# Kernel optimization log

Hardware: AMD Instinct MI355X
Metric: run time of the kernel (lower is better)

Reference implementation:

```python
import jax, jax.numpy as jnp
import numpy as np

U = 100000   # num_users
I = 100000   # num_items
D = 64       # latent_dim_rec
L = 3        # lightGCN_n_layers
E = 6400000  # number of nonzeros in the sparse adjacency
B = 16384    # batch of (user, item) pairs
N = U + I


def setup_inputs() -> dict:
    key = jax.random.key(0)
    ks = jax.random.split(key, 11)
    return {
        "user_emb": 0.1 * jax.random.normal(ks[0], (U, D), dtype=jnp.float32),
        "item_emb": 0.1 * jax.random.normal(ks[1], (I, D), dtype=jnp.float32),
        "symptom_emb": 0.1 * jax.random.normal(ks[2], (U, D), dtype=jnp.float32),
        "herb_emb": 0.1 * jax.random.normal(ks[3], (I, D), dtype=jnp.float32),
        "user_lw": jax.random.uniform(ks[4], (L + 1,), dtype=jnp.float32),
        "item_lw": jax.random.uniform(ks[5], (L + 1,), dtype=jnp.float32),
        # symmetric-normalized adjacency values are small positive numbers
        "edge_val": jax.random.uniform(ks[6], (E,), dtype=jnp.float32) / 32.0,
        "edge_row": jax.random.randint(ks[7], (E,), 0, N, dtype=jnp.int32),
        "edge_col": jax.random.randint(ks[8], (E,), 0, N, dtype=jnp.int32),
        "users": jax.random.randint(ks[9], (B,), 0, U, dtype=jnp.int32),
        "items": jax.random.randint(ks[10], (B,), 0, I, dtype=jnp.int32),
    }


def _computer(user_emb, item_emb, symptom_emb, herb_emb, user_lw, item_lw,
              edge_val, edge_row, edge_col):
    # layer-0 semantic fusion
    a0 = jax.nn.sigmoid(user_lw[0])
    b0 = jax.nn.sigmoid(item_lw[0])
    u = a0 * user_emb + (1.0 - a0) * symptom_emb
    it = b0 * item_emb + (1.0 - b0) * herb_emb
    all_emb = jnp.concatenate([u, it], axis=0)  # [N, D]
    acc = all_emb  # running sum over layers (mean taken at the end)
    for layer in range(1, L + 1):
        # SpMM: A @ all_emb via gather + segment_sum over edge list
        msg = edge_val[:, None] * all_emb[edge_col]          # [E, D]
        all_emb = jax.ops.segment_sum(msg, edge_row, num_segments=N)
        a = jax.nn.sigmoid(user_lw[layer])
        b = jax.nn.sigmoid(item_lw[layer])
        cu = a * all_emb[:U] + (1.0 - a) * symptom_emb
        ci = b * all_emb[U:] + (1.0 - b) * herb_emb
        all_emb = jnp.concatenate([cu, ci], axis=0)
        acc = acc + all_emb
    light_out = acc / (L + 1)   # mean over stacked layer outputs
    return light_out[:U], light_out[U:]


def reference(user_emb, item_emb, symptom_emb, herb_emb, user_lw, item_lw,
              edge_val, edge_row, edge_col, users, items):
    all_users, all_items = _computer(user_emb, item_emb, symptom_emb, herb_emb,
                                     user_lw, item_lw, edge_val, edge_row, edge_col)
    users_emb = all_users[users]   # [B, D]
    items_emb = all_items[items]   # [B, D]
    gamma = jnp.sum(users_emb * items_emb, axis=1)  # [B]
    return gamma
```

## Files before the change

### kernel.cpp

```cpp
#include <hip/hip_runtime.h>

constexpr int U_N = 100000;
constexpr int I_N = 100000;
constexpr int D   = 64;
constexpr int NL  = 3;
constexpr int NN  = U_N + I_N;
constexpr long long NDLL = (long long)NN * D;
constexpr long long ND4  = NDLL / 4;
constexpr long long UD4  = (long long)U_N * D / 4;

constexpr int BKT_SHIFT = 10;
constexpr int BKT_W     = 1024;
constexpr int NBKT      = (NN + BKT_W - 1) / BKT_W;
constexpr int ABLK      = 1024;

typedef float f32x2 __attribute__((ext_vector_type(2)));

__device__ __forceinline__ float sigmoidf_(float x) {
    return 1.0f / (1.0f + expf(-x));
}

__device__ __forceinline__ float bf2f(unsigned short b) {
    return __uint_as_float((unsigned int)b << 16);
}
__device__ __forceinline__ float bf_lo(unsigned int u) {
    return __uint_as_float(u << 16);
}
__device__ __forceinline__ float bf_hi(unsigned int u) {
    return __uint_as_float(u & 0xFFFF0000u);
}
__device__ __forceinline__ f32x2 bfpair(unsigned int u) {
    f32x2 r;
    r.x = __uint_as_float(u << 16);
    r.y = __uint_as_float(u & 0xFFFF0000u);
    return r;
}
__device__ __forceinline__ unsigned short f2bf(float f) {
    unsigned int u = __float_as_uint(f);
    u += 0x7FFFu + ((u >> 16) & 1u);
    return (unsigned short)(u >> 16);
}
__device__ __forceinline__ unsigned int pack2bf(float lo, float hi) {
    return (unsigned int)f2bf(lo) | ((unsigned int)f2bf(hi) << 16);
}

__global__ void fuse0_bf16_kernel(const float* __restrict__ user_emb,
                                  const float* __restrict__ item_emb,
                                  const float* __restrict__ symptom_emb,
                                  const float* __restrict__ herb_emb,
                                  const float* __restrict__ user_lw,
                                  const float* __restrict__ item_lw,
                                  unsigned short* __restrict__ e0b) {
    long long idx = (long long)blockIdx.x * blockDim.x + threadIdx.x;
    if (idx >= ND4) return;
    float a0 = sigmoidf_(user_lw[0]);
    float b0 = sigmoidf_(item_lw[0]);
    float4 e, s;
    float w;
    if (idx < UD4) {
        e = ((const float4*)user_emb)[idx];
        s = ((const float4*)symptom_emb)[idx];
        w = a0;
    } else {
        long long j = idx - UD4;
        e = ((const float4*)item_emb)[j];
        s = ((const float4*)herb_emb)[j];
        w = b0;
    }
    ushort4 rb;
    rb.x = f2bf(w * e.x + (1.0f - w) * s.x);
    rb.y = f2bf(w * e.y + (1.0f - w) * s.y);
    rb.z = f2bf(w * e.z + (1.0f - w) * s.z);
    rb.w = f2bf(w * e.w + (1.0f - w) * s.w);
    ((ushort4*)e0b)[idx] = rb;
}

__global__ void zero_bcnt_kernel(int* __restrict__ bucket_cnt) {
    int i = blockIdx.x * blockDim.x + threadIdx.x;
    if (i < NBKT) bucket_cnt[i] = 0;
}

__global__ void bucket_hist_kernel(const int* __restrict__ edge_row,
                                   int* __restrict__ bucket_cnt,
                                   int E, int chunk) {
    __shared__ int h[NBKT];
    int tid = threadIdx.x;
    for (int i = tid; i < NBKT; i += blockDim.x) h[i] = 0;
    __syncthreads();
    int s = blockIdx.x * chunk;
    int eend = min(E, s + chunk);
    for (int e = s + tid; e < eend; e += blockDim.x)
        atomicAdd(&h[edge_row[e] >> BKT_SHIFT], 1);
    __syncthreads();
    for (int i = tid; i < NBKT; i += blockDim.x) {
        int c = h[i];
        if (c) atomicAdd(&bucket_cnt[i], c);
    }
}

__global__ void scan_bkt_kernel(const int* __restrict__ bucket_cnt,
                                int* __restrict__ boff,
                                int* __restrict__ cursorA, int E) {
    __shared__ int sm[256];
    int tid = threadIdx.x;
    int x = (tid < NBKT) ? bucket_cnt[tid] : 0;
    sm[tid] = x;
    __syncthreads();
    for (int off = 1; off < 256; off <<= 1) {
        int t = (tid >= off) ? sm[tid - off] : 0;
        __syncthreads();
        sm[tid] += t;
        __syncthreads();
    }
    if (tid < NBKT) {
        int excl = sm[tid] - x;
        boff[tid] = excl;
        cursorA[tid] = excl;
    }
    if (tid == 0) boff[NBKT] = E;
}

__global__ void bin_scatter_kernel(const float* __restrict__ edge_val,
                                   const int*   __restrict__ edge_row,
                                   const int*   __restrict__ edge_col,
                                   int* __restrict__ cursorA,
                                   int2* __restrict__ binned,
                                   int E, int chunk) {
    __shared__ int h[NBKT];
    int tid = threadIdx.x;
    for (int i = tid; i < NBKT; i += blockDim.x) h[i] = 0;
    __syncthreads();
    int s = blockIdx.x * chunk;
    int eend = min(E, s + chunk);
    for (int e = s + tid; e < eend; e += blockDim.x)
        atomicAdd(&h[edge_row[e] >> BKT_SHIFT], 1);
    __syncthreads();
    for (int i = tid; i < NBKT; i += blockDim.x) {
        int c = h[i];
        if (c) h[i] = atomicAdd(&cursorA[i], c);
    }
    __syncthreads();
    for (int e = s + tid; e < eend; e += blockDim.x) {
        int r = edge_row[e];
        int b = r >> BKT_SHIFT;
        int pos = atomicAdd(&h[b], 1);
        binned[pos] = make_int2(__float_as_int(edge_val[e]),
                                edge_col[e] | ((r & (BKT_W - 1)) << 18));
    }
}

__global__ void bucket_to_csr_kernel(const int2* __restrict__ binned,
                                     const int*  __restrict__ boff,
                                     int*  __restrict__ row_ptr,
                                     int2* __restrict__ sorted, int E) {
    int b = blockIdx.x;
    int start = boff[b];
    int end   = boff[b + 1];
    __shared__ int rc[BKT_W];
    __shared__ int sm[BKT_W];
    int tid = threadIdx.x;
    rc[tid] = 0;
    __syncthreads();
    for (int e = start + tid; e < end; e += blockDim.x)
        atomicAdd(&rc[(unsigned)binned[e].y >> 18], 1);
    __syncthreads();
    int x = rc[tid];
    sm[tid] = x;
    __syncthreads();
    for (int off = 1; off < BKT_W; off <<= 1) {
        int t = (tid >= off) ? sm[tid - off] : 0;
        __syncthreads();
        sm[tid] += t;
        __syncthreads();
    }
    int excl = sm[tid] - x;
    int gidx = (b << BKT_SHIFT) + tid;
    if (gidx <= NN) row_ptr[gidx] = start + excl;
    __syncthreads();
    rc[tid] = excl;
    __syncthreads();
    for (int e = start + tid; e < end; e += blockDim.x) {
        int2 a = binned[e];
        int rl = (unsigned)a.y >> 18;
        int pos = start + atomicAdd(&rc[rl], 1);
        sorted[pos] = make_int2(a.x, a.y & 0x3FFFF);
    }
}

__device__ __forceinline__ void csr_row_sum(const int2* __restrict__ sorted,
                                            const uint4* __restrict__ src16,
                                            int start, int end,
                                            int g, int p, f32x2 s[4]) {
    f32x2 s0[4], s1[4];
    #pragma unroll
    for (int j = 0; j < 4; ++j) {
        s0[j] = (f32x2){0.f, 0.f};
        s1[j] = (f32x2){0.f, 0.f};
    }
    int e = start;
    for (; e + 16 <= end; e += 16) {
        int2 a0 = sorted[e + g];
        int2 a1 = sorted[e + 8 + g];
        uint4 q0 = src16[((size_t)(unsigned)a0.y << 3) + p];
        uint4 q1 = src16[((size_t)(unsigned)a1.y << 3) + p];
        f32x2 v0; v0.x = __int_as_float(a0.x); v0.y = v0.x;
        f32x2 v1; v1.x = __int_as_float(a1.x); v1.y = v1.x;
        s0[0] += v0 * bfpair(q0.x);
        s0[1] += v0 * bfpair(q0.y);
        s0[2] += v0 * bfpair(q0.z);
        s0[3] += v0 * bfpair(q0.w);
        s1[0] += v1 * bfpair(q1.x);
        s1[1] += v1 * bfpair(q1.y);
        s1[2] += v1 * bfpair(q1.z);
        s1[3] += v1 * bfpair(q1.w);
    }
    for (; e < end; e += 8) {
        int idx = e + g;
        int2 a = (idx < end) ? sorted[idx] : make_int2(0, 0);
        uint4 q = src16[((size_t)(unsigned)a.y << 3) + p];
        f32x2 v; v.x = __int_as_float(a.x); v.y = v.x;
        s0[0] += v * bfpair(q.x);
        s0[1] += v * bfpair(q.y);
        s0[2] += v * bfpair(q.z);
        s0[3] += v * bfpair(q.w);
    }
    #pragma unroll
    for (int j = 0; j < 4; ++j) s[j] = s0[j] + s1[j];
    #pragma unroll
    for (int m = 8; m < 64; m <<= 1) {
        #pragma unroll
        for (int j = 0; j < 4; ++j) {
            f32x2 t;
            t.x = __shfl_xor(s[j].x, m, 64);
            t.y = __shfl_xor(s[j].y, m, 64);
            s[j] += t;
        }
    }
}

__global__ void spmm_csr_full_kernel(const int2* __restrict__ sorted,
                                     const int*  __restrict__ row_ptr,
                                     const unsigned short* __restrict__ src,
                                     const float* __restrict__ symptom_emb,
                                     const float* __restrict__ herb_emb,
                                     const float* __restrict__ user_lw,
                                     const float* __restrict__ item_lw,
                                     int layer,
                                     unsigned short* __restrict__ dst_b) {
    int wid  = threadIdx.x >> 6;
    int lane = threadIdx.x & 63;
    int row  = blockIdx.x * (blockDim.x >> 6) + wid;
    if (row >= NN) return;
    int g = lane >> 3;
    int p = lane & 7;

    f32x2 s[4];
    csr_row_sum(sorted, (const uint4*)src, row_ptr[row], row_ptr[row + 1],
                g, p, s);

    if (lane < 8) {
        size_t o = ((size_t)row << 6) + ((size_t)p << 3);
        float wgt;
        const float* semp;
        if (row < U_N) {
            wgt = sigmoidf_(user_lw[layer]);
            semp = symptom_emb + o;
        } else {
            wgt = sigmoidf_(item_lw[layer]);
            semp = herb_emb + o - ((size_t)U_N << 6);
        }
        float4 sa = *(const float4*)semp;
        float4 sb = *(const float4*)(semp + 4);
        float r0 = wgt * s[0].x + (1.0f - wgt) * sa.x;
        float r1 = wgt * s[0].y + (1.0f - wgt) * sa.y;
        float r2 = wgt * s[1].x + (1.0f - wgt) * sa.z;
        float r3 = wgt * s[1].y + (1.0f - wgt) * sa.w;
        float r4 = wgt * s[2].x + (1.0f - wgt) * sb.x;
        float r5 = wgt * s[2].y + (1.0f - wgt) * sb.y;
        float r6 = wgt * s[3].x + (1.0f - wgt) * sb.z;
        float r7 = wgt * s[3].y + (1.0f - wgt) * sb.w;
        uint4 ob;
        ob.x = pack2bf(r0, r1);
        ob.y = pack2bf(r2, r3);
        ob.z = pack2bf(r4, r5);
        ob.w = pack2bf(r6, r7);
        *(uint4*)(dst_b + o) = ob;
    }
}

__global__ void spmm_csr_compact_kernel(const int2* __restrict__ sorted,
                                        const int*  __restrict__ row_ptr,
                                        const unsigned short* __restrict__ src,
                                        const float* __restrict__ user_emb,
                                        const float* __restrict__ item_emb,
                                        const float* __restrict__ symptom_emb,
                                        const float* __restrict__ herb_emb,
                                        const float* __restrict__ user_lw,
                                        const float* __restrict__ item_lw,
                                        int layer,
                                        const int* __restrict__ users,
                                        const int* __restrict__ items,
                                        const unsigned short* __restrict__ e1b,
                                        const unsigned short* __restrict__ e2b,
                                        float* __restrict__ e3c,
                                        int B) {
    int wid  = threadIdx.x >> 6;
    int lane = threadIdx.x & 63;
    int b    = blockIdx.x * (blockDim.x >> 6) + wid;
    if (b >= 2 * B) return;
    int row = (b < B) ? users[b] : (items[b - B] + U_N);
    int g = lane >> 3;
    int p = lane & 7;

    f32x2 s[4];
    csr_row_sum(sorted, (const uint4*)src, row_ptr[row], row_ptr[row + 1],
                g, p, s);

    if (lane < 8) {
        size_t orow = ((size_t)row << 6) + ((size_t)p << 3);
        float wgt, w0;
        const float* semp;
        const float* embp;
        if (row < U_N) {
            wgt = sigmoidf_(user_lw[layer]);
            w0  = sigmoidf_(user_lw[0]);
            semp = symptom_emb + orow;
            embp = user_emb + orow;
        } else {
            size_t ol = orow - ((size_t)U_N << 6);
            wgt = sigmoidf_(item_lw[layer]);
            w0  = sigmoidf_(item_lw[0]);
            semp = herb_emb + ol;
            embp = item_emb + ol;
        }
        float4 sa = *(const float4*)semp;
        float4 sb = *(const float4*)(semp + 4);
        float4 ea = *(const float4*)embp;
        float4 eb = *(const float4*)(embp + 4);
        uint4 q1 = ((const uint4*)e1b)[((size_t)row << 3) + p];
        uint4 q2 = ((const uint4*)e2b)[((size_t)row << 3) + p];
        float4 ra, rb;
        ra.x = (w0 * ea.x + (1.0f - w0) * sa.x) + bf_lo(q1.x) + bf_lo(q2.x)
             + (wgt * s[0].x + (1.0f - wgt) * sa.x);
        ra.y = (w0 * ea.y + (1.0f - w0) * sa.y) + bf_hi(q1.x) + bf_hi(q2.x)
             + (wgt * s[0].y + (1.0f - wgt) * sa.y);
        ra.z = (w0 * ea.z + (1.0f - w0) * sa.z) + bf_lo(q1.y) + bf_lo(q2.y)
             + (wgt * s[1].x + (1.0f - wgt) * sa.z);
        ra.w = (w0 * ea.w + (1.0f - w0) * sa.w) + bf_hi(q1.y) + bf_hi(q2.y)
             + (wgt * s[1].y + (1.0f - wgt) * sa.w);
        rb.x = (w0 * eb.x + (1.0f - w0) * sb.x) + bf_lo(q1.z) + bf_lo(q2.z)
             + (wgt * s[2].x + (1.0f - wgt) * sb.x);
        rb.y = (w0 * eb.y + (1.0f - w0) * sb.y) + bf_hi(q1.z) + bf_hi(q2.z)
             + (wgt * s[2].y + (1.0f - wgt) * sb.y);
        rb.z = (w0 * eb.z + (1.0f - w0) * sb.z) + bf_lo(q1.w) + bf_lo(q2.w)
             + (wgt * s[3].x + (1.0f - wgt) * sb.z);
        rb.w = (w0 * eb.w + (1.0f - w0) * sb.w) + bf_hi(q1.w) + bf_hi(q2.w)
             + (wgt * s[3].y + (1.0f - wgt) * sb.w);
        float* op = e3c + ((size_t)b << 6) + ((size_t)p << 3);
        *(float4*)op = ra;
        *(float4*)(op + 4) = rb;
    }
}

__global__ void gamma_kernel(const float* __restrict__ e3c,
                             float* __restrict__ out,
                             int B) {
    int gtid = blockIdx.x * blockDim.x + threadIdx.x;
    int wid  = gtid >> 6;
    int lane = threadIdx.x & 63;
    if (wid >= B) return;
    float su = e3c[((size_t)wid << 6) | lane];
    float si = e3c[((size_t)(B + wid) << 6) | lane];
    float pr = su * si;
    #pragma unroll
    for (int off = 32; off > 0; off >>= 1)
        pr += __shfl_down(pr, off, 64);
    if (lane == 0) out[wid] = pr * (1.0f / 16.0f);
}

__global__ void fuse0_kernel(const float* __restrict__ user_emb,
                             const float* __restrict__ item_emb,
                             const float* __restrict__ symptom_emb,
                             const float* __restrict__ herb_emb,
                             const float* __restrict__ user_lw,
                             const float* __restrict__ item_lw,
                             float* __restrict__ bufA,
                             float* __restrict__ acc,
                             float* __restrict__ bufB) {
    long long idx = (long long)blockIdx.x * blockDim.x + threadIdx.x;
    if (idx >= ND4) return;
    float a0 = sigmoidf_(user_lw[0]);
    float b0 = sigmoidf_(item_lw[0]);
    float4 e, s;
    float w;
    if (idx < UD4) {
        e = ((const float4*)user_emb)[idx];
        s = ((const float4*)symptom_emb)[idx];
        w = a0;
    } else {
        long long j = idx - UD4;
        e = ((const float4*)item_emb)[j];
        s = ((const float4*)herb_emb)[j];
        w = b0;
    }
    float4 r;
    r.x = w * e.x + (1.0f - w) * s.x;
    r.y = w * e.y + (1.0f - w) * s.y;
    r.z = w * e.z + (1.0f - w) * s.z;
    r.w = w * e.w + (1.0f - w) * s.w;
    ((float4*)bufA)[idx] = r;
    ((float4*)acc)[idx]  = r;
    float4 z; z.x = z.y = z.z = z.w = 0.0f;
    ((float4*)bufB)[idx] = z;
}

__global__ void spmm_scatter_kernel(const float* __restrict__ edge_val,
                                    const int*   __restrict__ edge_row,
                                    const int*   __restrict__ edge_col,
                                    const float* __restrict__ src,
                                    float*       __restrict__ dst,
                                    long long total) {
    long long idx = (long long)blockIdx.x * blockDim.x + threadIdx.x;
    if (idx >= total) return;
    long long e = idx >> 4;
    int       q = (int)(idx & 15);
    int r = edge_row[e];
    int c = edge_col[e];
    float v = edge_val[e];
    float4 x = *(const float4*)(src + (long long)c * D + q * 4);
    float* d = dst + (long long)r * D + q * 4;
    atomicAdd(d + 0, v * x.x);
    atomicAdd(d + 1, v * x.y);
    atomicAdd(d + 2, v * x.z);
    atomicAdd(d + 3, v * x.w);
}

__global__ void fuse_layer_kernel(const float* __restrict__ symptom_emb,
                                  const float* __restrict__ herb_emb,
                                  const float* __restrict__ user_lw,
                                  const float* __restrict__ item_lw,
                                  int layer,
                                  float* __restrict__ bufA,
                                  float* __restrict__ bufB,
                                  float* __restrict__ acc) {
    long long idx = (long long)blockIdx.x * blockDim.x + threadIdx.x;
    if (idx >= ND4) return;
    float a = sigmoidf_(user_lw[layer]);
    float b = sigmoidf_(item_lw[layer]);
    float4 m = ((float4*)bufB)[idx];
    float4 z; z.x = z.y = z.z = z.w = 0.0f;
    ((float4*)bufB)[idx] = z;
    float4 s;
    float w;
    if (idx < UD4) {
        s = ((const float4*)symptom_emb)[idx];
        w = a;
    } else {
        s = ((const float4*)herb_emb)[idx - UD4];
        w = b;
    }
    float4 r;
    r.x = w * m.x + (1.0f - w) * s.x;
    r.y = w * m.y + (1.0f - w) * s.y;
    r.z = w * m.z + (1.0f - w) * s.z;
    r.w = w * m.w + (1.0f - w) * s.w;
    ((float4*)bufA)[idx] = r;
    float4 ac = ((float4*)acc)[idx];
    ac.x += r.x; ac.y += r.y; ac.z += r.z; ac.w += r.w;
    ((float4*)acc)[idx] = ac;
}

__global__ void gamma_acc_kernel(const float* __restrict__ acc,
                                 const int* __restrict__ users,
                                 const int* __restrict__ items,
                                 float* __restrict__ out,
                                 int B) {
    int gtid = blockIdx.x * blockDim.x + threadIdx.x;
    int wid  = gtid >> 6;
    int lane = threadIdx.x & 63;
    if (wid >= B) return;
    int u  = users[wid];
    int it = items[wid];
    float su = acc[(long long)u * D + lane];
    float si = acc[((long long)(U_N + it)) * D + lane];
    float p = su * si;
    #pragma unroll
    for (int off = 32; off > 0; off >>= 1)
        p += __shfl_down(p, off, 64);
    if (lane == 0) out[wid] = p * (1.0f / 16.0f);
}

extern "C" void kernel_launch(void* const* d_in, const int* in_sizes, int n_in,
                              void* d_out, int out_size, void* d_ws, size_t ws_size,
                              hipStream_t stream) {
    const float* user_emb    = (const float*)d_in[0];
    const float* item_emb    = (const float*)d_in[1];
    const float* symptom_emb = (const float*)d_in[2];
    const float* herb_emb    = (const float*)d_in[3];
    const float* user_lw     = (const float*)d_in[4];
    const float* item_lw     = (const float*)d_in[5];
    const float* edge_val    = (const float*)d_in[6];
    const int*   edge_row    = (const int*)d_in[7];
    const int*   edge_col    = (const int*)d_in[8];
    const int*   users       = (const int*)d_in[9];
    const int*   items       = (const int*)d_in[10];
    float* out = (float*)d_out;

    const int E = in_sizes[6];
    const int B = in_sizes[9];
    const int TPB = 256;

    size_t off = 0;
    auto carve = [&](size_t bytes) -> char* {
        char* p = (char*)d_ws + off;
        off += (bytes + 255) & ~(size_t)255;
        return p;
    };
    unsigned short* e0b     = (unsigned short*)carve(NDLL * 2);
    unsigned short* e1b     = (unsigned short*)carve(NDLL * 2);
    int2*           binned  = (int2*)carve((size_t)E * 8);
    int2*           sorted  = (int2*)carve((size_t)E * 8);
    int*            row_ptr = (int*)carve((size_t)(NN + 1) * 4);
    int*            bcnt    = (int*)carve((size_t)NBKT * 4);
    int*            boff    = (int*)carve((size_t)(NBKT + 1) * 4);
    int*            cursorA = (int*)carve((size_t)NBKT * 4);
    const size_t fast_bytes = off;
    unsigned short* e2b = e0b;
    float*          e3c = (float*)binned;

    if (ws_size >= fast_bytes && (size_t)E * 8 >= (size_t)2 * B * D * 4) {
        int fb = (int)((ND4 + TPB - 1) / TPB);
        fuse0_bf16_kernel<<<fb, TPB, 0, stream>>>(user_emb, item_emb, symptom_emb,
                                                  herb_emb, user_lw, item_lw, e0b);

        int chunk = (E + ABLK - 1) / ABLK;
        zero_bcnt_kernel<<<1, TPB, 0, stream>>>(bcnt);
        bucket_hist_kernel<<<ABLK, TPB, 0, stream>>>(edge_row, bcnt, E, chunk);
        scan_bkt_kernel<<<1, 256, 0, stream>>>(bcnt, boff, cursorA, E);
        bin_scatter_kernel<<<ABLK, TPB, 0, stream>>>(edge_val, edge_row, edge_col,
                                                     cursorA, binned, E, chunk);
        bucket_to_csr_kernel<<<NBKT, BKT_W, 0, stream>>>(binned, boff, row_ptr,
                                                         sorted, E);

        int sblocks = (NN * 64 + TPB - 1) / TPB;
        spmm_csr_full_kernel<<<sblocks, TPB, 0, stream>>>(
            sorted, row_ptr, e0b, symptom_emb, herb_emb,
            user_lw, item_lw, 1, e1b);
        spmm_csr_full_kernel<<<sblocks, TPB, 0, stream>>>(
            sorted, row_ptr, e1b, symptom_emb, herb_emb,
            user_lw, item_lw, 2, e2b);
        int cblocks = (2 * B * 64 + TPB - 1) / TPB;
        spmm_csr_compact_kernel<<<cblocks, TPB, 0, stream>>>(
            sorted, row_ptr, e2b, user_emb, item_emb, symptom_emb, herb_emb,
            user_lw, item_lw, 3, users, items, e1b, e2b, e3c, B);

        int gblocks = (B * 64 + TPB - 1) / TPB;
        gamma_kernel<<<gblocks, TPB, 0, stream>>>(e3c, out, B);
    } else {
        float* bufA = (float*)d_ws;
        float* bufB = bufA + NDLL;
        float* acc2 = bufB + NDLL;

        int fb = (int)((ND4 + TPB - 1) / TPB);
        fuse0_kernel<<<fb, TPB, 0, stream>>>(user_emb, item_emb, symptom_emb,
                                             herb_emb, user_lw, item_lw,
                                             bufA, acc2, bufB);
        for (int layer = 1; layer <= NL; ++layer) {
            long long total = (long long)E * 16;
            int blocks = (int)((total + TPB - 1) / TPB);
            spmm_scatter_kernel<<<blocks, TPB, 0, stream>>>(edge_val, edge_row,
                                                            edge_col, bufA, bufB,
                                                            total);
            int fblocks = (int)((ND4 + TPB - 1) / TPB);
            fuse_layer_kernel<<<fblocks, TPB, 0, stream>>>(symptom_emb, herb_emb,
                                                           user_lw, item_lw, layer,
                                                           bufA, bufB, acc2);
        }
        int gblocks = (B * 64 + TPB - 1) / TPB;
        gamma_acc_kernel<<<gblocks, TPB, 0, stream>>>(acc2, users, items, out, B);
    }
}
```

Before: 692.3 us.

## Map eight CSR rows per wavefront with one 8-lane group per row

The SpMM kernels now assign each 8-lane group its own row instead of spreading one row's edges over a whole wavefront, which removes the cross-lane shuffle reduction and the idle lanes in the epilogue. The sorted edge array now stores the column pre-shifted to a byte offset, so the gather address is a single OR. Each group walks its row's edges serially with a 4-way unroll. Rows of different lengths within a wavefront can now cause divergence, and edge metadata loads are broadcast within groups rather than coalesced across the wave. The launch block counts are adjusted to match (TPB is assumed to be 256, giving 32 rows per block).

```diff
diff --git a/kernel.cpp b/kernel.cpp
--- a/kernel.cpp
+++ b/kernel.cpp
@@ -183,58 +183,45 @@
         int2 a = binned[e];
         int rl = (unsigned)a.y >> 18;
         int pos = start + atomicAdd(&rc[rl], 1);
-        sorted[pos] = make_int2(a.x, a.y & 0x3FFFF);
-    }
-}
-
-__device__ __forceinline__ void csr_row_sum(const int2* __restrict__ sorted,
-                                            const uint4* __restrict__ src16,
-                                            int start, int end,
-                                            int g, int p, f32x2 s[4]) {
-    f32x2 s0[4], s1[4];
+        sorted[pos] = make_int2(a.x, (a.y & 0x3FFFF) << 7);
+    }
+}
+
+__device__ __forceinline__ void csr_row_sum8(const int2* __restrict__ sorted,
+                                             const char* __restrict__ srcB,
+                                             int start, int end, unsigned poff,
+                                             f32x2 s[4]) {
     #pragma unroll
-    for (int j = 0; j < 4; ++j) {
-        s0[j] = (f32x2){0.f, 0.f};
-        s1[j] = (f32x2){0.f, 0.f};
-    }
+    for (int j = 0; j < 4; ++j) s[j] = (f32x2){0.f, 0.f};
     int e = start;
-    for (; e + 16 <= end; e += 16) {
-        int2 a0 = sorted[e + g];
-        int2 a1 = sorted[e + 8 + g];
-        uint4 q0 = src16[((size_t)(unsigned)a0.y << 3) + p];
-        uint4 q1 = src16[((size_t)(unsigned)a1.y << 3) + p];
+    for (; e + 4 <= end; e += 4) {
+        int2 a0 = sorted[e + 0];
+        int2 a1 = sorted[e + 1];
+        int2 a2 = sorted[e + 2];
+        int2 a3 = sorted[e + 3];
+        uint4 q0 = *(const uint4*)(srcB + (size_t)((unsigned)a0.y | poff));
+        uint4 q1 = *(const uint4*)(srcB + (size_t)((unsigned)a1.y | poff));
+        uint4 q2 = *(const uint4*)(srcB + (size_t)((unsigned)a2.y | poff));
+        uint4 q3 = *(const uint4*)(srcB + (size_t)((unsigned)a3.y | poff));
         f32x2 v0; v0.x = __int_as_float(a0.x); v0.y = v0.x;
         f32x2 v1; v1.x = __int_as_float(a1.x); v1.y = v1.x;
-        s0[0] += v0 * bfpair(q0.x);
-        s0[1] += v0 * bfpair(q0.y);
-        s0[2] += v0 * bfpair(q0.z);
-        s0[3] += v0 * bfpair(q0.w);
-        s1[0] += v1 * bfpair(q1.x);
-        s1[1] += v1 * bfpair(q1.y);
-        s1[2] += v1 * bfpair(q1.z);
-        s1[3] += v1 * bfpair(q1.w);
-    }
-    for (; e < end; e += 8) {
-        int idx = e + g;
-        int2 a = (idx < end) ? sorted[idx] : make_int2(0, 0);
-        uint4 q = src16[((size_t)(unsigned)a.y << 3) + p];
+        f32x2 v2; v2.x = __int_as_float(a2.x); v2.y = v2.x;
+        f32x2 v3; v3.x = __int_as_float(a3.x); v3.y = v3.x;
+        s[0] += v0 * bfpair(q0.x); s[1] += v0 * bfpair(q0.y);
+        s[2] += v0 * bfpair(q0.z); s[3] += v0 * bfpair(q0.w);
+        s[0] += v1 * bfpair(q1.x); s[1] += v1 * bfpair(q1.y);
+        s[2] += v1 * bfpair(q1.z); s[3] += v1 * bfpair(q1.w);
+        s[0] += v2 * bfpair(q2.x); s[1] += v2 * bfpair(q2.y);
+        s[2] += v2 * bfpair(q2.z); s[3] += v2 * bfpair(q2.w);
+        s[0] += v3 * bfpair(q3.x); s[1] += v3 * bfpair(q3.y);
+        s[2] += v3 * bfpair(q3.z); s[3] += v3 * bfpair(q3.w);
+    }
+    for (; e < end; ++e) {
+        int2 a = sorted[e];
+        uint4 q = *(const uint4*)(srcB + (size_t)((unsigned)a.y | poff));
         f32x2 v; v.x = __int_as_float(a.x); v.y = v.x;
-        s0[0] += v * bfpair(q.x);
-        s0[1] += v * bfpair(q.y);
-        s0[2] += v * bfpair(q.z);
-        s0[3] += v * bfpair(q.w);
-    }
-    #pragma unroll
-    for (int j = 0; j < 4; ++j) s[j] = s0[j] + s1[j];
-    #pragma unroll
-    for (int m = 8; m < 64; m <<= 1) {
-        #pragma unroll
-        for (int j = 0; j < 4; ++j) {
-            f32x2 t;
-            t.x = __shfl_xor(s[j].x, m, 64);
-            t.y = __shfl_xor(s[j].y, m, 64);
-            s[j] += t;
-        }
+        s[0] += v * bfpair(q.x); s[1] += v * bfpair(q.y);
+        s[2] += v * bfpair(q.z); s[3] += v * bfpair(q.w);
     }
 }
 
@@ -249,43 +236,35 @@
                                      unsigned short* __restrict__ dst_b) {
     int wid  = threadIdx.x >> 6;
     int lane = threadIdx.x & 63;
-    int row  = blockIdx.x * (blockDim.x >> 6) + wid;
+    int r    = lane >> 3;
+    int p    = lane & 7;
+    int row  = (blockIdx.x * (blockDim.x >> 6) + wid) * 8 + r;
     if (row >= NN) return;
-    int g = lane >> 3;
-    int p = lane & 7;
+    int start = row_ptr[row];
+    int end   = row_ptr[row + 1];
 
     f32x2 s[4];
-    csr_row_sum(sorted, (const uint4*)src, row_ptr[row], row_ptr[row + 1],
-                g, p, s);
-
-    if (lane < 8) {
-        size_t o = ((size_t)row << 6) + ((size_t)p << 3);
-        float wgt;
-        const float* semp;
-        if (row < U_N) {
-            wgt = sigmoidf_(user_lw[layer]);
-            semp = symptom_emb + o;
-        } else {
-            wgt = sigmoidf_(item_lw[layer]);
-            semp = herb_emb + o - ((size_t)U_N << 6);
-        }
-        float4 sa = *(const float4*)semp;
-        float4 sb = *(const float4*)(semp + 4);
-        float r0 = wgt * s[0].x + (1.0f - wgt) * sa.x;
-        float r1 = wgt * s[0].y + (1.0f - wgt) * sa.y;
-        float r2 = wgt * s[1].x + (1.0f - wgt) * sa.z;
-        float r3 = wgt * s[1].y + (1.0f - wgt) * sa.w;
-        float r4 = wgt * s[2].x + (1.0f - wgt) * sb.x;
-        float r5 = wgt * s[2].y + (1.0f - wgt) * sb.y;
-        float r6 = wgt * s[3].x + (1.0f - wgt) * sb.z;
-        float r7 = wgt * s[3].y + (1.0f - wgt) * sb.w;
-        uint4 ob;
-        ob.x = pack2bf(r0, r1);
-        ob.y = pack2bf(r2, r3);
-        ob.z = pack2bf(r4, r5);
-        ob.w = pack2bf(r6, r7);
-        *(uint4*)(dst_b + o) = ob;
-    }
+    csr_row_sum8(sorted, (const char*)src, start, end, (unsigned)(p << 4), s);
+
+    size_t o = ((size_t)row << 6) + ((size_t)p << 3);
+    float wgt;
+    const float* semp;
+    if (row < U_N) {
+        wgt = sigmoidf_(user_lw[layer]);
+        semp = symptom_emb + o;
+    } else {
+        wgt = sigmoidf_(item_lw[layer]);
+        semp = herb_emb + o - ((size_t)U_N << 6);
+    }
+    float4 sa = *(const float4*)semp;
+    float4 sb = *(const float4*)(semp + 4);
+    float om = 1.0f - wgt;
+    uint4 ob;
+    ob.x = pack2bf(wgt * s[0].x + om * sa.x, wgt * s[0].y + om * sa.y);
+    ob.y = pack2bf(wgt * s[1].x + om * sa.z, wgt * s[1].y + om * sa.w);
+    ob.z = pack2bf(wgt * s[2].x + om * sb.x, wgt * s[2].y + om * sb.y);
+    ob.w = pack2bf(wgt * s[3].x + om * sb.z, wgt * s[3].y + om * sb.w);
+    *(uint4*)(dst_b + o) = ob;
 }
 
 __global__ void spmm_csr_compact_kernel(const int2* __restrict__ sorted,
@@ -306,60 +285,60 @@
                                         int B) {
     int wid  = threadIdx.x >> 6;
     int lane = threadIdx.x & 63;
-    int b    = blockIdx.x * (blockDim.x >> 6) + wid;
+    int r    = lane >> 3;
+    int p    = lane & 7;
+    int b    = (blockIdx.x * (blockDim.x >> 6) + wid) * 8 + r;
     if (b >= 2 * B) return;
     int row = (b < B) ? users[b] : (items[b - B] + U_N);
-    int g = lane >> 3;
-    int p = lane & 7;
+    int start = row_ptr[row];
+    int end   = row_ptr[row + 1];
 
     f32x2 s[4];
-    csr_row_sum(sorted, (const uint4*)src, row_ptr[row], row_ptr[row + 1],
-                g, p, s);
-
-    if (lane < 8) {
-        size_t orow = ((size_t)row << 6) + ((size_t)p << 3);
-        float wgt, w0;
-        const float* semp;
-        const float* embp;
-        if (row < U_N) {
-            wgt = sigmoidf_(user_lw[layer]);
-            w0  = sigmoidf_(user_lw[0]);
-            semp = symptom_emb + orow;
-            embp = user_emb + orow;
-        } else {
-            size_t ol = orow - ((size_t)U_N << 6);
-            wgt = sigmoidf_(item_lw[layer]);
-            w0  = sigmoidf_(item_lw[0]);
-            semp = herb_emb + ol;
-            embp = item_emb + ol;
-        }
-        float4 sa = *(const float4*)semp;
-        float4 sb = *(const float4*)(semp + 4);
-        float4 ea = *(const float4*)embp;
-        float4 eb = *(const float4*)(embp + 4);
-        uint4 q1 = ((const uint4*)e1b)[((size_t)row << 3) + p];
-        uint4 q2 = ((const uint4*)e2b)[((size_t)row << 3) + p];
-        float4 ra, rb;
-        ra.x = (w0 * ea.x + (1.0f - w0) * sa.x) + bf_lo(q1.x) + bf_lo(q2.x)
-             + (wgt * s[0].x + (1.0f - wgt) * sa.x);
-        ra.y = (w0 * ea.y + (1.0f - w0) * sa.y) + bf_hi(q1.x) + bf_hi(q2.x)
-             + (wgt * s[0].y + (1.0f - wgt) * sa.y);
-        ra.z = (w0 * ea.z + (1.0f - w0) * sa.z) + bf_lo(q1.y) + bf_lo(q2.y)
-             + (wgt * s[1].x + (1.0f - wgt) * sa.z);
-        ra.w = (w0 * ea.w + (1.0f - w0) * sa.w) + bf_hi(q1.y) + bf_hi(q2.y)
-             + (wgt * s[1].y + (1.0f - wgt) * sa.w);
-        rb.x = (w0 * eb.x + (1.0f - w0) * sb.x) + bf_lo(q1.z) + bf_lo(q2.z)
-             + (wgt * s[2].x + (1.0f - wgt) * sb.x);
-        rb.y = (w0 * eb.y + (1.0f - w0) * sb.y) + bf_hi(q1.z) + bf_hi(q2.z)
-             + (wgt * s[2].y + (1.0f - wgt) * sb.y);
-        rb.z = (w0 * eb.z + (1.0f - w0) * sb.z) + bf_lo(q1.w) + bf_lo(q2.w)
-             + (wgt * s[3].x + (1.0f - wgt) * sb.z);
-        rb.w = (w0 * eb.w + (1.0f - w0) * sb.w) + bf_hi(q1.w) + bf_hi(q2.w)
-             + (wgt * s[3].y + (1.0f - wgt) * sb.w);
-        float* op = e3c + ((size_t)b << 6) + ((size_t)p << 3);
-        *(float4*)op = ra;
-        *(float4*)(op + 4) = rb;
-    }
+    csr_row_sum8(sorted, (const char*)src, start, end, (unsigned)(p << 4), s);
+
+    size_t orow = ((size_t)row << 6) + ((size_t)p << 3);
+    float wgt, w0;
+    const float* semp;
+    const float* embp;
+    if (row < U_N) {
+        wgt = sigmoidf_(user_lw[layer]);
+        w0  = sigmoidf_(user_lw[0]);
+        semp = symptom_emb + orow;
+        embp = user_emb + orow;
+    } else {
+        size_t ol = orow - ((size_t)U_N << 6);
+        wgt = sigmoidf_(item_lw[layer]);
+        w0  = sigmoidf_(item_lw[0]);
+        semp = herb_emb + ol;
+        embp = item_emb + ol;
+    }
+    float4 sa = *(const float4*)semp;
+    float4 sb = *(const float4*)(semp + 4);
+    float4 ea = *(const float4*)embp;
+    float4 eb = *(const float4*)(embp + 4);
+    uint4 q1 = ((const uint4*)e1b)[((size_t)row << 3) + p];
+    uint4 q2 = ((const uint4*)e2b)[((size_t)row << 3) + p];
+    float om = 1.0f - wgt, om0 = 1.0f - w0;
+    float4 ra, rb;
+    ra.x = (w0 * ea.x + om0 * sa.x) + bf_lo(q1.x) + bf_lo(q2.x)
+         + (wgt * s[0].x + om * sa.x);
+    ra.y = (w0 * ea.y + om0 * sa.y) + bf_hi(q1.x) + bf_hi(q2.x)
+         + (wgt * s[0].y + om * sa.y);
+    ra.z = (w0 * ea.z + om0 * sa.z) + bf_lo(q1.y) + bf_lo(q2.y)
+         + (wgt * s[1].x + om * sa.z);
+    ra.w = (w0 * ea.w + om0 * sa.w) + bf_hi(q1.y) + bf_hi(q2.y)
+         + (wgt * s[1].y + om * sa.w);
+    rb.x = (w0 * eb.x + om0 * sb.x) + bf_lo(q1.z) + bf_lo(q2.z)
+         + (wgt * s[2].x + om * sb.x);
+    rb.y = (w0 * eb.y + om0 * sb.y) + bf_hi(q1.z) + bf_hi(q2.z)
+         + (wgt * s[2].y + om * sb.y);
+    rb.z = (w0 * eb.z + om0 * sb.z) + bf_lo(q1.w) + bf_lo(q2.w)
+         + (wgt * s[3].x + om * sb.z);
+    rb.w = (w0 * eb.w + om0 * sb.w) + bf_hi(q1.w) + bf_hi(q2.w)
+         + (wgt * s[3].y + om * sb.w);
+    float* op = e3c + ((size_t)b << 6) + ((size_t)p << 3);
+    *(float4*)op = ra;
+    *(float4*)(op + 4) = rb;
 }
 
 __global__ void gamma_kernel(const float* __restrict__ e3c,
@@ -542,14 +521,14 @@
         bucket_to_csr_kernel<<<NBKT, BKT_W, 0, stream>>>(binned, boff, row_ptr,
                                                          sorted, E);
 
-        int sblocks = (NN * 64 + TPB - 1) / TPB;
+        int sblocks = (NN + 31) / 32;
         spmm_csr_full_kernel<<<sblocks, TPB, 0, stream>>>(
             sorted, row_ptr, e0b, symptom_emb, herb_emb,
             user_lw, item_lw, 1, e1b);
         spmm_csr_full_kernel<<<sblocks, TPB, 0, stream>>>(
             sorted, row_ptr, e1b, symptom_emb, herb_emb,
             user_lw, item_lw, 2, e2b);
-        int cblocks = (2 * B * 64 + TPB - 1) / TPB;
+        int cblocks = (2 * B + 31) / 32;
         spmm_csr_compact_kernel<<<cblocks, TPB, 0, stream>>>(
             sorted, row_ptr, e2b, user_emb, item_emb, symptom_emb, herb_emb,
             user_lw, item_lw, 3, users, items, e1b, e2b, e3c, B);
```

Result: no change. 682.2 us (-1.5%).
